# Kernel optimization log

Hardware: AMD Instinct MI355X
Metric: run time of the kernel (lower is better)

The kernel has to match this reference:

```python
import jax, jax.numpy as jnp
import numpy as np

N, L, H, E, V, PAD = 128, 64, 512, 512, 32000, 0


def setup_inputs() -> dict:
    key = jax.random.key(0)
    ks = jax.random.split(key, 8)
    s_in = 1.0 / np.sqrt(E)
    s_sani = 1.0 / np.sqrt(2 * H)
    s_out = 1.0 / np.sqrt(H)
    labels = jax.random.randint(ks[0], (N, L), 0, V)
    emb_table = jax.random.normal(ks[1], (V, E), jnp.float32) * 0.02
    emb_table = emb_table.at[PAD].set(0.0)  # padding_idx row is zero-initialized
    W_in = jax.random.uniform(ks[2], (H, E), jnp.float32, -s_in, s_in)
    b_in = jax.random.uniform(ks[3], (H,), jnp.float32, -s_in, s_in)
    W_sani = jax.random.uniform(ks[4], (H, 2 * H), jnp.float32, -s_sani, s_sani)
    b_sani = jax.random.uniform(ks[5], (H,), jnp.float32, -s_sani, s_sani)
    W_out = jax.random.uniform(ks[6], (E, H), jnp.float32, -s_out, s_out)
    b_out = jax.random.uniform(ks[7], (E,), jnp.float32, -s_out, s_out)
    return dict(labels=labels, emb_table=emb_table, W_in=W_in, b_in=b_in,
                W_sani=W_sani, b_sani=b_sani, W_out=W_out, b_out=b_out)


def reference(labels, emb_table, W_in, b_in, W_sani, b_sani, W_out, b_out):
    n, l = labels.shape
    emb = emb_table[labels]                                   # [N,L,E]
    x = jnp.einsum('nle,he->nlh', emb, W_in) + b_in           # [N,L,H] input conversion
    h_dim = W_in.shape[0]

    def step(states, sc):
        s, h0 = sc                                            # h0: [N,H]
        def body(li, carry):
            h, st = carry
            prev = st[li]                                     # hiddenStateLast[li]
            new_h = jnp.concatenate([prev, h], axis=-1) @ W_sani.T + b_sani
            take = li < s                                     # triangular mask
            return (jnp.where(take, new_h, h),
                    st.at[li].set(jnp.where(take, h, prev)))
        h, states = jax.lax.fori_loop(0, l, body, (h0, states))
        states = states.at[s].set(h)                          # hiddenStateLast[s] = h
        return states, h                                      # outputStates[s] = h

    states0 = jnp.zeros((l, n, h_dim), x.dtype)
    _, outs = jax.lax.scan(step, states0, (jnp.arange(l), jnp.swapaxes(x, 0, 1)))
    # torch: pt.concat(outputStates, dim=0) -> [L*N, H], outputLayer, reshape(N,L,E)
    y = outs.reshape(l * n, h_dim) @ W_out.T + b_out
    y = y.reshape(n, l, E)  # faithful to the original (sequence-major) reshape
    # CrossEntropyLoss with float (probability) targets: classes along dim 1 (L)
    logp = jax.nn.log_softmax(y, axis=1)
    loss = -(emb * logp).sum(axis=1).mean()
    return loss
```

## Files before the change

### kernel.cpp

```cpp
#include <hip/hip_runtime.h>
#include <hip/hip_bf16.h>

typedef __attribute__((ext_vector_type(8))) short short8;
typedef __attribute__((ext_vector_type(4))) float floatx4;

#define NB 128
#define LS 64
#define HD 512
#define ED 512
#define NH 65536
#define LDA 72
#define LDC 136

#define OFF_WIN    0ull
#define OFF_WOUT   524288ull
#define OFF_XT     1048576ull
#define OFF_LVL0   9437184ull
#define OFF_LVL1   17825792ull
#define OFF_OUTS   26214400ull
#define OFF_PA     34603008ull
#define OFF_PB     39845888ull
#define OFF_BCAT   45088768ull
#define OFF_BETA   52428800ull
#define OFF_PART   52436992ull
#define OFF_WSHI   52437504ull
#define OFF_WSLO   53486080ull
#define OFF_PHI    54534656ull
#define OFF_PLO    57156096ull
#define OFF_Y      OFF_LVL0

static __device__ __forceinline__ unsigned short f2b(float f) {
  unsigned u = __float_as_uint(f);
  u += 0x7fffu + ((u >> 16) & 1u);
  return (unsigned short)(u >> 16);
}
static __device__ __forceinline__ float b2f(unsigned short h) {
  return __uint_as_float(((unsigned)h) << 16);
}

static __device__ __forceinline__ void gl_lds16(const unsigned short* g, unsigned short* l) {
  __builtin_amdgcn_global_load_lds(
      (const __attribute__((address_space(1))) void*)g,
      (__attribute__((address_space(3))) void*)l, 16, 0, 0);
}

static __device__ __forceinline__ uint4 cvt8hi(const float* s) {
  floatx4 f0 = *(const floatx4*)s;
  floatx4 f1 = *(const floatx4*)(s + 4);
  float f[8] = {f0.x, f0.y, f0.z, f0.w, f1.x, f1.y, f1.z, f1.w};
  unsigned short b[8];
#pragma unroll
  for (int k = 0; k < 8; ++k) b[k] = f2b(f[k]);
  uint4 u;
  u.x = b[0] | ((unsigned)b[1] << 16); u.y = b[2] | ((unsigned)b[3] << 16);
  u.z = b[4] | ((unsigned)b[5] << 16); u.w = b[6] | ((unsigned)b[7] << 16);
  return u;
}

__device__ __forceinline__ void gemm_core24(const unsigned short* As, const unsigned short* Bs,
                                            floatx4 acc[2][4], int wm, int wn, int lane) {
  const int rb = lane & 15;
  const int kg = (lane >> 4) * 8;
#pragma unroll
  for (int kk = 0; kk < 64; kk += 32) {
    short8 a[2], b[4];
#pragma unroll
    for (int i = 0; i < 2; ++i)
      a[i] = *(const short8*)&As[(wm * 32 + i * 16 + rb) * LDA + kk + kg];
#pragma unroll
    for (int j = 0; j < 4; ++j)
      b[j] = *(const short8*)&Bs[(wn * 64 + j * 16 + rb) * LDA + kk + kg];
#pragma unroll
    for (int i = 0; i < 2; ++i)
#pragma unroll
      for (int j = 0; j < 4; ++j)
        acc[i][j] = __builtin_amdgcn_mfma_f32_16x16x32_bf16(a[i], b[j], acc[i][j], 0, 0, 0);
  }
}

__device__ __forceinline__ void gemm_core64s(const unsigned short* As, const unsigned short* Bs,
                                             floatx4 acc[2][4], int wm, int wn, int lane) {
  const int rb = lane & 15;
  const int kg = (lane >> 4) * 8;
  const int xv = (rb & 7) * 8;
#pragma unroll
  for (int kk = 0; kk < 64; kk += 32) {
    const int co = (kk + kg) ^ xv;
    short8 a[2], b[4];
#pragma unroll
    for (int i = 0; i < 2; ++i)
      a[i] = *(const short8*)&As[(wm * 32 + i * 16 + rb) * 64 + co];
#pragma unroll
    for (int j = 0; j < 4; ++j)
      b[j] = *(const short8*)&Bs[(wn * 64 + j * 16 + rb) * 64 + co];
#pragma unroll
    for (int i = 0; i < 2; ++i)
#pragma unroll
      for (int j = 0; j < 4; ++j)
        acc[i][j] = __builtin_amdgcn_mfma_f32_16x16x32_bf16(a[i], b[j], acc[i][j], 0, 0, 0);
  }
}

__device__ __forceinline__ void stageA_bf16(unsigned short* As, const unsigned short* src, int tid) {
  int r = tid >> 3, kc = (tid & 7) * 8;
#pragma unroll
  for (int p = 0; p < 2; ++p)
    *(uint4*)&As[(r + p * 32) * LDA + kc] = *(const uint4*)(src + (size_t)(r + p * 32) * 512 + kc);
}

__device__ __forceinline__ void stageA_emb(unsigned short* As, const float* table,
                                           const int* labels, int m0, int k0, int tid) {
  int r = tid >> 3, kc = (tid & 7) * 8;
#pragma unroll
  for (int p = 0; p < 2; ++p) {
    int row = r + p * 32;
    const float* s = table + (size_t)labels[m0 + row] * ED + k0 + kc;
    *(uint4*)&As[row * LDA + kc] = cvt8hi(s);
  }
}

__device__ __forceinline__ void stageB(unsigned short* Bs, const unsigned short* src, int ldB, int tid) {
  int r = tid >> 3, kc = (tid & 7) * 8;
#pragma unroll
  for (int p = 0; p < 4; ++p)
    *(uint4*)&Bs[(r + p * 32) * LDA + kc] = *(const uint4*)(src + (size_t)(r + p * 32) * ldB + kc);
}

__global__ __launch_bounds__(256) void k_gemm_emb(const float* __restrict__ table,
                                                  const int* __restrict__ labels,
                                                  const unsigned short* __restrict__ Wb,
                                                  const float* __restrict__ bias,
                                                  unsigned short* __restrict__ xt) {
  __shared__ unsigned short As[64 * LDA];
  __shared__ unsigned short Bs[128 * LDA];
  int tid = threadIdx.x;
  int mtile = blockIdx.x >> 2, ntile = blockIdx.x & 3;
  int m0 = mtile * 64, n0 = ntile * 128;
  int lane = tid & 63, wave = tid >> 6, wm = wave >> 1, wn = wave & 1;
  floatx4 acc[2][4] = {};
  for (int k0 = 0; k0 < 512; k0 += 64) {
    stageA_emb(As, table, labels, m0, k0, tid);
    stageB(Bs, Wb + (size_t)n0 * 512 + k0, 512, tid);
    __syncthreads();
    gemm_core24(As, Bs, acc, wm, wn, lane);
    __syncthreads();
  }
  int rb = lane & 15, rg = (lane >> 4) * 4;
#pragma unroll
  for (int i = 0; i < 2; ++i)
#pragma unroll
    for (int j = 0; j < 4; ++j) {
      int col = n0 + wn * 64 + j * 16 + rb;
      float bv = bias[col];
#pragma unroll
      for (int reg = 0; reg < 4; ++reg) {
        int m = m0 + wm * 32 + i * 16 + rg + reg;
        int n = m >> 6, l = m & 63;
        xt[((size_t)l * NB + n) * HD + col] = f2b(acc[i][j][reg] + bv);
      }
    }
}

__global__ __launch_bounds__(256) void k_cvtWs(const float* __restrict__ Ws,
                                               unsigned short* __restrict__ Hi,
                                               unsigned short* __restrict__ Lo) {
  int i = blockIdx.x * 256 + threadIdx.x;
  const float* s = Ws + (size_t)i * 8;
  unsigned short hb[8], lb[8];
#pragma unroll
  for (int k = 0; k < 8; ++k) {
    float f = s[k];
    unsigned short H = f2b(f);
    hb[k] = H; lb[k] = f2b(f - b2f(H));
  }
  uint4 h, l;
  h.x = hb[0] | ((unsigned)hb[1] << 16); h.y = hb[2] | ((unsigned)hb[3] << 16);
  h.z = hb[4] | ((unsigned)hb[5] << 16); h.w = hb[6] | ((unsigned)hb[7] << 16);
  l.x = lb[0] | ((unsigned)lb[1] << 16); l.y = lb[2] | ((unsigned)lb[3] << 16);
  l.z = lb[4] | ((unsigned)lb[5] << 16); l.w = lb[6] | ((unsigned)lb[7] << 16);
  *(uint4*)(Hi + (size_t)i * 8) = h;
  *(uint4*)(Lo + (size_t)i * 8) = l;
}

__global__ __launch_bounds__(256) void k_cvtP(const float* __restrict__ P,
                                              unsigned short* __restrict__ Hi,
                                              unsigned short* __restrict__ Lo, int n8) {
  int i = blockIdx.x * 256 + threadIdx.x;
  if (i >= n8) return;
  const float* s = P + (size_t)i * 8;
  unsigned short hb[8], lb[8];
#pragma unroll
  for (int k = 0; k < 8; ++k) {
    float f = s[k];
    unsigned short H = f2b(f);
    hb[k] = H; lb[k] = f2b(f - b2f(H));
  }
  uint4 h, l;
  h.x = hb[0] | ((unsigned)hb[1] << 16); h.y = hb[2] | ((unsigned)hb[3] << 16);
  h.z = hb[4] | ((unsigned)hb[5] << 16); h.w = hb[6] | ((unsigned)hb[7] << 16);
  l.x = lb[0] | ((unsigned)lb[1] << 16); l.y = lb[2] | ((unsigned)lb[3] << 16);
  l.z = lb[4] | ((unsigned)lb[5] << 16); l.w = lb[6] | ((unsigned)lb[7] << 16);
  *(uint4*)(Hi + (size_t)i * 8) = h;
  *(uint4*)(Lo + (size_t)i * 8) = l;
}

__global__ __launch_bounds__(256) void k_coef(const unsigned short* __restrict__ Phi,
                                              const unsigned short* __restrict__ Plo,
                                              float* __restrict__ Pout,
                                              const unsigned short* __restrict__ WsHi,
                                              const unsigned short* __restrict__ WsLo,
                                              int m) {
  __shared__ unsigned short As[64 * LDA];
  __shared__ unsigned short Bs[128 * LDA];
  int tid = threadIdx.x;
  int j = blockIdx.x >> 5, tile = blockIdx.x & 31;
  int k0r = (tile >> 2) * 64, n0 = (tile & 3) * 128;
  int lane = tid & 63, wave = tid >> 6, wm = wave >> 1, wn = wave & 1;
  floatx4 acc[2][4] = {};
  for (int term = 0; term < 2; ++term) {
    if (term == 0 && j > m) continue;
    if (term == 1 && j < 1) continue;
    const size_t pbase = (size_t)(term == 0 ? j : j - 1) * 262144;
    const int coloff = (term == 0) ? 512 : 0;
    for (int v = 0; v < 3; ++v) {
      const unsigned short* Asrc = (v == 2 ? Plo : Phi) + pbase;
      const unsigned short* Bsrc = (v == 1 ? WsLo : WsHi);
      for (int t0 = 0; t0 < 512; t0 += 64) {
        stageA_bf16(As, Asrc + (size_t)k0r * 512 + t0, tid);
        stageB(Bs, Bsrc + (size_t)n0 * 1024 + coloff + t0, 1024, tid);
        __syncthreads();
        gemm_core24(As, Bs, acc, wm, wn, lane);
        __syncthreads();
      }
    }
  }
  int rb = lane & 15, rg = (lane >> 4) * 4;
#pragma unroll
  for (int i = 0; i < 2; ++i)
#pragma unroll
    for (int jj = 0; jj < 4; ++jj) {
      int col = n0 + wn * 64 + jj * 16 + rb;
#pragma unroll
      for (int reg = 0; reg < 4; ++reg) {
        int row = wm * 32 + i * 16 + rg + reg;
        Pout[(size_t)j * 262144 + (size_t)(k0r + row) * 512 + col] = acc[i][jj][reg];
      }
    }
}

__global__ __launch_bounds__(256) void k_trW(const float* __restrict__ Ws,
                                             float* __restrict__ P1) {
  __shared__ float t[64][65];
  int mat = blockIdx.x >> 6, tile = blockIdx.x & 63;
  int a0 = (tile >> 3) * 64, b0 = (tile & 7) * 64;
  int coloff = (mat == 0) ? 512 : 0;
  for (int pp = 0; pp < 16; ++pp) {
    int idx = pp * 256 + threadIdx.x, rr = idx >> 6, cc = idx & 63;
    t[rr][cc] = Ws[(size_t)(b0 + rr) * 1024 + coloff + a0 + cc];
  }
  __syncthreads();
  for (int pp = 0; pp < 16; ++pp) {
    int idx = pp * 256 + threadIdx.x, rr = idx >> 6, cc = idx & 63;
    P1[(size_t)mat * 262144 + (size_t)(a0 + rr) * 512 + b0 + cc] = t[cc][rr];
  }
}

__global__ __launch_bounds__(256) void k_trB(const float* __restrict__ Pr,
                                             unsigned short* __restrict__ Bout,
                                             int r) {
  __shared__ float t[64][65];
  int q = blockIdx.x >> 6, tile = blockIdx.x & 63;
  int t0 = (tile >> 3) * 64, i0 = (tile & 7) * 64;
  const float* P = Pr + (size_t)(r - q) * 262144;
  int ldB = (r + 1) * 512;
  for (int pp = 0; pp < 16; ++pp) {
    int idx = pp * 256 + threadIdx.x, rr = idx >> 6, cc = idx & 63;
    t[rr][cc] = P[(size_t)(t0 + rr) * 512 + i0 + cc];
  }
  __syncthreads();
  for (int pp = 0; pp < 16; ++pp) {
    int idx = pp * 256 + threadIdx.x, rr = idx >> 6, cc = idx & 63;
    Bout[(size_t)(i0 + rr) * ldB + q * 512 + t0 + cc] = f2b(t[cc][rr]);
  }
}

__global__ __launch_bounds__(64) void k_bias_step(const float* __restrict__ Ws,
                                                  const float* __restrict__ b,
                                                  const float* __restrict__ bprev,
                                                  float* __restrict__ bout) {
  int i = blockIdx.x, t = threadIdx.x;
  float p = 0.f;
  for (int k = t; k < 512; k += 64)
    p += (Ws[(size_t)i * 1024 + k] + Ws[(size_t)i * 1024 + 512 + k]) * bprev[k];
#pragma unroll
  for (int off = 32; off > 0; off >>= 1) p += __shfl_down(p, off, 64);
  if (t == 0) bout[i] = p + b[i];
}

__global__ __launch_bounds__(256) void k_step(const unsigned short* __restrict__ src,
                                              unsigned short* __restrict__ dst,
                                              unsigned short* __restrict__ outs,
                                              const unsigned short* __restrict__ Bcat,
                                              const float* __restrict__ beta,
                                              int L_prev, int m, int nmain, int g) {
  __shared__ unsigned short lds[24576];
  unsigned short* const A0 = lds;
  unsigned short* const A1 = lds + 4096;
  unsigned short* const B0 = lds + 8192;
  unsigned short* const B1 = lds + 16384;
  const int tid = threadIdx.x, bid = blockIdx.x;
  const int mainWG = 32 * g;
  int r, s, nb0, n0;
  if (bid < mainWG) {
    const int xcd = bid & 7, w = bid >> 3;
    const int sgrp = xcd >> 1, ngrp = xcd & 1;
    const int s_rel = sgrp * g + (w >> 2);
    if (s_rel >= nmain) return;
    const int sub2 = w & 3;
    nb0 = (sub2 >> 1) * 64;
    n0 = (ngrp * 2 + (sub2 & 1)) * 128;
    r = m; s = L_prev + m + s_rel;
  } else {
    const int db = bid - mainWG;
    r = 1 + (db >> 3);
    const int sub = db & 7;
    nb0 = (sub >> 2) * 64; n0 = (sub & 3) * 128;
    s = L_prev + r;
  }
  const int ldB = (r + 1) * 512;
  const unsigned short* Bp = Bcat + (size_t)262144 * (((r - 1) * (r + 2)) >> 1);
  const unsigned short* abase = src + (size_t)(s - r) * NH + (size_t)nb0 * HD;
  const float* bet = beta + (size_t)(r - 1) * 512;
  const int nk = (r + 1) * 8;
  const int lane = tid & 63, wave = tid >> 6, wm = wave >> 1, wn = wave & 1;
  const int rr_ = tid >> 3;
  const int kcs = (((tid & 7) ^ ((tid >> 3) & 7))) * 8;

  floatx4 acc[2][4] = {};

#define STAGE(Ab, Bb, kcol)                                                          \
  { int q_ = (kcol) >> 9, ac_ = (kcol) & 511;                                        \
    const unsigned short* a0_ = abase + (size_t)q_ * NH + ac_;                       \
    unsigned short* lA = (Ab) + (tid >> 6) * 512;                                    \
    unsigned short* lB = (Bb) + (tid >> 6) * 512;                                    \
    gl_lds16(a0_ + (size_t)rr_ * HD + kcs, lA);                                      \
    gl_lds16(a0_ + (size_t)(rr_ + 32) * HD + kcs, lA + 2048);                        \
    gl_lds16(Bp + (size_t)(n0 + rr_) * ldB + (kcol) + kcs, lB);                      \
    gl_lds16(Bp + (size_t)(n0 + rr_ + 32) * ldB + (kcol) + kcs, lB + 2048);          \
    gl_lds16(Bp + (size_t)(n0 + rr_ + 64) * ldB + (kcol) + kcs, lB + 4096);          \
    gl_lds16(Bp + (size_t)(n0 + rr_ + 96) * ldB + (kcol) + kcs, lB + 6144); }

  STAGE(A0, B0, 0)
  __syncthreads();
  for (int k = 0; k < nk; k += 2) {
    if (k + 1 < nk) STAGE(A1, B1, (k + 1) * 64)
    gemm_core64s(A0, B0, acc, wm, wn, lane);
    __syncthreads();
    if (k + 2 < nk) STAGE(A0, B0, (k + 2) * 64)
    gemm_core64s(A1, B1, acc, wm, wn, lane);
    __syncthreads();
  }
#undef STAGE

  unsigned short* Ct = lds;
  const int rbc = lane & 15, rg = (lane >> 4) * 4;
#pragma unroll
  for (int i = 0; i < 2; ++i)
#pragma unroll
    for (int j = 0; j < 4; ++j) {
      int col = wn * 64 + j * 16 + rbc;
      float bv = bet[n0 + col];
#pragma unroll
      for (int reg = 0; reg < 4; ++reg) {
        int row = wm * 32 + i * 16 + rg + reg;
        Ct[row * LDC + col] = f2b(acc[i][j][reg] + bv);
      }
    }
  __syncthreads();
  const bool wdst = (r == m);
  const bool wout = (r < m) || (s == L_prev + m);
  unsigned short* d1 = dst  + (size_t)s * NH + (size_t)nb0 * HD + n0;
  unsigned short* d2 = outs + (size_t)s * NH + (size_t)nb0 * HD + n0;
  const int lrow = tid >> 4, lcol = (tid & 15) * 8;
#pragma unroll
  for (int sweep = 0; sweep < 4; ++sweep) {
    int row = sweep * 16 + lrow;
    uint4 v = *(const uint4*)&Ct[row * LDC + lcol];
    if (wdst) *(uint4*)(d1 + (size_t)row * HD + lcol) = v;
    if (wout) *(uint4*)(d2 + (size_t)row * HD + lcol) = v;
  }
}

__global__ __launch_bounds__(256) void k_gemm_out(const unsigned short* __restrict__ outs,
                                                  const unsigned short* __restrict__ Wb,
                                                  const float* __restrict__ bias,
                                                  float* __restrict__ Y) {
  __shared__ unsigned short As[64 * LDA];
  __shared__ unsigned short Bs[128 * LDA];
  int tid = threadIdx.x;
  int mtile = blockIdx.x >> 2, ntile = blockIdx.x & 3;
  int m0 = mtile * 64, n0 = ntile * 128;
  int lane = tid & 63, wave = tid >> 6, wm = wave >> 1, wn = wave & 1;
  floatx4 acc[2][4] = {};
  for (int k0 = 0; k0 < 512; k0 += 64) {
    stageA_bf16(As, outs + (size_t)m0 * 512 + k0, tid);
    stageB(Bs, Wb + (size_t)n0 * 512 + k0, 512, tid);
    __syncthreads();
    gemm_core24(As, Bs, acc, wm, wn, lane);
    __syncthreads();
  }
  int rb = lane & 15, rg = (lane >> 4) * 4;
#pragma unroll
  for (int i = 0; i < 2; ++i)
#pragma unroll
    for (int j = 0; j < 4; ++j) {
      int col = n0 + wn * 64 + j * 16 + rb;
      float bv = bias[col];
#pragma unroll
      for (int reg = 0; reg < 4; ++reg) {
        int row = m0 + wm * 32 + i * 16 + rg + reg;
        Y[(size_t)row * 512 + col] = acc[i][j][reg] + bv;
      }
    }
}

__global__ __launch_bounds__(256) void k_cvtw(const float* __restrict__ Win,
                                              const float* __restrict__ Wsani,
                                              const float* __restrict__ Wout,
                                              unsigned short* __restrict__ dWin,
                                              unsigned short* __restrict__ dBcat1,
                                              unsigned short* __restrict__ dWout) {
  int i = blockIdx.x * 256 + threadIdx.x;
  const float* src;
  unsigned short* dst;
  int off;
  if (i < 65536)       { src = Win;   dst = dWin;   off = i; }
  else if (i < 196608) { src = Wsani; dst = dBcat1; off = i - 65536; }
  else                 { src = Wout;  dst = dWout;  off = i - 196608; }
  floatx4 v = *(const floatx4*)(src + (size_t)off * 4);
  uint2 u;
  u.x = (unsigned)f2b(v.x) | ((unsigned)f2b(v.y) << 16);
  u.y = (unsigned)f2b(v.z) | ((unsigned)f2b(v.w) << 16);
  *(uint2*)(dst + (size_t)off * 4) = u;
}

__global__ void k_copy(const uint4* __restrict__ src, uint4* __restrict__ dst, int n) {
  int i = blockIdx.x * blockDim.x + threadIdx.x;
  if (i < n) dst[i] = src[i];
}

__global__ __launch_bounds__(256) void k_loss(const float* __restrict__ Y,
                                              const float* __restrict__ table,
                                              const int* __restrict__ labels,
                                              float* __restrict__ partials) {
  int n = blockIdx.x, tid = threadIdx.x;
  float total = 0.f;
#pragma unroll
  for (int e2 = 0; e2 < 2; ++e2) {
    int e = e2 * 256 + tid;
    float mx = -1e30f;
    for (int l = 0; l < 64; ++l)
      mx = fmaxf(mx, Y[(size_t)(n * 64 + l) * 512 + e]);
    float se = 0.f;
    for (int l = 0; l < 64; ++l)
      se += expf(Y[(size_t)(n * 64 + l) * 512 + e] - mx);
    float lse = mx + logf(se);
    for (int l = 0; l < 64; ++l) {
      float embv = table[(size_t)labels[n * 64 + l] * ED + e];
      total += embv * (Y[(size_t)(n * 64 + l) * 512 + e] - lse);
    }
  }
  __shared__ float red[256];
  red[tid] = total;
  __syncthreads();
  for (int s2 = 128; s2 > 0; s2 >>= 1) {
    if (tid < s2) red[tid] += red[tid + s2];
    __syncthreads();
  }
  if (tid == 0) partials[n] = red[0];
}

__global__ void k_final(const float* __restrict__ partials, float* __restrict__ out) {
  if (threadIdx.x == 0) {
    double s = 0.0;
    for (int i = 0; i < 128; ++i) s += (double)partials[i];
    out[0] = (float)(-s / 65536.0);
  }
}

extern "C" void kernel_launch(void* const* d_in, const int* in_sizes, int n_in,
                              void* d_out, int out_size, void* d_ws, size_t ws_size,
                              hipStream_t stream) {
  const int*   labels = (const int*)d_in[0];
  const float* table  = (const float*)d_in[1];
  const float* W_in   = (const float*)d_in[2];
  const float* b_in   = (const float*)d_in[3];
  const float* W_sani = (const float*)d_in[4];
  const float* b_sani = (const float*)d_in[5];
  const float* W_out  = (const float*)d_in[6];
  const float* b_out  = (const float*)d_in[7];

  char* ws = (char*)d_ws;
  unsigned short* Win_b  = (unsigned short*)(ws + OFF_WIN);
  unsigned short* Wout_b = (unsigned short*)(ws + OFF_WOUT);
  unsigned short* xt     = (unsigned short*)(ws + OFF_XT);
  unsigned short* lvl0   = (unsigned short*)(ws + OFF_LVL0);
  unsigned short* lvl1   = (unsigned short*)(ws + OFF_LVL1);
  unsigned short* outs   = (unsigned short*)(ws + OFF_OUTS);
  float*          Pa     = (float*)(ws + OFF_PA);
  float*          Pb     = (float*)(ws + OFF_PB);
  unsigned short* Bcat   = (unsigned short*)(ws + OFF_BCAT);
  float*          beta   = (float*)(ws + OFF_BETA);
  float*          parts  = (float*)(ws + OFF_PART);
  unsigned short* WsHi   = (unsigned short*)(ws + OFF_WSHI);
  unsigned short* WsLo   = (unsigned short*)(ws + OFF_WSLO);
  unsigned short* PHi    = (unsigned short*)(ws + OFF_PHI);
  unsigned short* PLo    = (unsigned short*)(ws + OFF_PLO);
  float*          Y      = (float*)(ws + OFF_Y);

  k_cvtw<<<1024, 256, 0, stream>>>(W_in, W_sani, W_out, Win_b, Bcat, Wout_b);
  k_cvtWs<<<256, 256, 0, stream>>>(W_sani, WsHi, WsLo);
  k_gemm_emb<<<512, 256, 0, stream>>>(table, labels, Win_b, b_in, xt);
  k_copy<<<32, 256, 0, stream>>>((const uint4*)xt, (uint4*)outs, 8192);

  k_copy<<<1, 128, 0, stream>>>((const uint4*)b_sani, (uint4*)beta, 128);
  k_bias_step<<<512, 64, 0, stream>>>(W_sani, b_sani, beta,        beta + 512);
  k_bias_step<<<512, 64, 0, stream>>>(W_sani, b_sani, beta + 512,  beta + 1024);
  k_bias_step<<<512, 64, 0, stream>>>(W_sani, b_sani, beta + 1024, beta + 1536);

  k_trW <<<128, 256, 0, stream>>>(W_sani, Pa);
  k_cvtP<<<256, 256, 0, stream>>>(Pa, PHi, PLo, 65536);
  k_coef<<< 96, 256, 0, stream>>>(PHi, PLo, Pb, WsHi, WsLo, 1);
  k_cvtP<<<384, 256, 0, stream>>>(Pb, PHi, PLo, 98304);
  k_trB <<<192, 256, 0, stream>>>(Pb, Bcat + 524288, 2);
  k_coef<<<128, 256, 0, stream>>>(PHi, PLo, Pa, WsHi, WsLo, 2);
  k_cvtP<<<512, 256, 0, stream>>>(Pa, PHi, PLo, 131072);
  k_trB <<<256, 256, 0, stream>>>(Pa, Bcat + 1310720, 3);
  k_coef<<<160, 256, 0, stream>>>(PHi, PLo, Pb, WsHi, WsLo, 3);
  k_trB <<<320, 256, 0, stream>>>(Pb, Bcat + 2359296, 4);

  const unsigned short* srcp = xt;
  for (int j = 1; j <= 16; ++j) {
    int L_prev = 4 * (j - 1);
    int m = (j == 16) ? 3 : 4;
    int nmain = 64 - (L_prev + m);
    int g = (nmain + 3) >> 2;
    unsigned short* dstp = ((j - 1) & 1) ? lvl1 : lvl0;
    k_step<<<32 * g + (m - 1) * 8, 256, 0, stream>>>(srcp, dstp, outs, Bcat, beta,
                                                     L_prev, m, nmain, g);
    srcp = dstp;
  }

  k_gemm_out<<<512, 256, 0, stream>>>(outs, Wout_b, b_out, Y);
  k_loss<<<128, 256, 0, stream>>>(Y, table, labels, parts);
  k_final<<<1, 64, 0, stream>>>(parts, (float*)d_out);
}
```

Baseline: 628.7 us.

## Fuse precompute conversions, double-buffer coef and output GEMMs, merge bias kernels

Folds the hi/lo bf16 split of W_sani into the weight-conversion kernel and produces hi/lo P matrices directly in k_trW and k_coef epilogues, which removes the separate k_cvtWs and k_cvtP launches and the fp32 P round trips. WsHi is now read from Bcat. The three bias-step launches are merged into one single-block kernel. k_coef and k_gemm_out now stage tiles with double-buffered direct global-to-LDS loads and a swizzled core, and the output GEMM writes Y through an LDS-staged coalesced epilogue. This cuts launch count and memory traffic in the setup phase, but the single-block bias kernel runs serially.

```diff
diff --git a/kernel.cpp b/kernel.cpp
--- a/kernel.cpp
+++ b/kernel.cpp
@@ -11,6 +11,7 @@
 #define NH 65536
 #define LDA 72
 #define LDC 136
+#define LDCF 132
 
 #define OFF_WIN    0ull
 #define OFF_WOUT   524288ull
@@ -18,15 +19,14 @@
 #define OFF_LVL0   9437184ull
 #define OFF_LVL1   17825792ull
 #define OFF_OUTS   26214400ull
-#define OFF_PA     34603008ull
-#define OFF_PB     39845888ull
+#define OFF_PHA    34603008ull
+#define OFF_PLA    37224448ull
+#define OFF_PHB    39845888ull
+#define OFF_PLB    42467328ull
 #define OFF_BCAT   45088768ull
 #define OFF_BETA   52428800ull
 #define OFF_PART   52436992ull
-#define OFF_WSHI   52437504ull
-#define OFF_WSLO   53486080ull
-#define OFF_PHI    54534656ull
-#define OFF_PLO    57156096ull
+#define OFF_WSLO   52437504ull
 #define OFF_Y      OFF_LVL0
 
 static __device__ __forceinline__ unsigned short f2b(float f) {
@@ -99,13 +99,6 @@
       for (int j = 0; j < 4; ++j)
         acc[i][j] = __builtin_amdgcn_mfma_f32_16x16x32_bf16(a[i], b[j], acc[i][j], 0, 0, 0);
   }
-}
-
-__device__ __forceinline__ void stageA_bf16(unsigned short* As, const unsigned short* src, int tid) {
-  int r = tid >> 3, kc = (tid & 7) * 8;
-#pragma unroll
-  for (int p = 0; p < 2; ++p)
-    *(uint4*)&As[(r + p * 32) * LDA + kc] = *(const uint4*)(src + (size_t)(r + p * 32) * 512 + kc);
 }
 
 __device__ __forceinline__ void stageA_emb(unsigned short* As, const float* table,
@@ -161,95 +154,44 @@
     }
 }
 
-__global__ __launch_bounds__(256) void k_cvtWs(const float* __restrict__ Ws,
-                                               unsigned short* __restrict__ Hi,
-                                               unsigned short* __restrict__ Lo) {
+__global__ __launch_bounds__(256) void k_cvtw(const float* __restrict__ Win,
+                                              const float* __restrict__ Wsani,
+                                              const float* __restrict__ Wout,
+                                              unsigned short* __restrict__ dWin,
+                                              unsigned short* __restrict__ dBcat1,
+                                              unsigned short* __restrict__ dWsLo,
+                                              unsigned short* __restrict__ dWout) {
   int i = blockIdx.x * 256 + threadIdx.x;
-  const float* s = Ws + (size_t)i * 8;
-  unsigned short hb[8], lb[8];
-#pragma unroll
-  for (int k = 0; k < 8; ++k) {
-    float f = s[k];
-    unsigned short H = f2b(f);
-    hb[k] = H; lb[k] = f2b(f - b2f(H));
-  }
-  uint4 h, l;
-  h.x = hb[0] | ((unsigned)hb[1] << 16); h.y = hb[2] | ((unsigned)hb[3] << 16);
-  h.z = hb[4] | ((unsigned)hb[5] << 16); h.w = hb[6] | ((unsigned)hb[7] << 16);
-  l.x = lb[0] | ((unsigned)lb[1] << 16); l.y = lb[2] | ((unsigned)lb[3] << 16);
-  l.z = lb[4] | ((unsigned)lb[5] << 16); l.w = lb[6] | ((unsigned)lb[7] << 16);
-  *(uint4*)(Hi + (size_t)i * 8) = h;
-  *(uint4*)(Lo + (size_t)i * 8) = l;
-}
-
-__global__ __launch_bounds__(256) void k_cvtP(const float* __restrict__ P,
-                                              unsigned short* __restrict__ Hi,
-                                              unsigned short* __restrict__ Lo, int n8) {
-  int i = blockIdx.x * 256 + threadIdx.x;
-  if (i >= n8) return;
-  const float* s = P + (size_t)i * 8;
-  unsigned short hb[8], lb[8];
-#pragma unroll
-  for (int k = 0; k < 8; ++k) {
-    float f = s[k];
-    unsigned short H = f2b(f);
-    hb[k] = H; lb[k] = f2b(f - b2f(H));
-  }
-  uint4 h, l;
-  h.x = hb[0] | ((unsigned)hb[1] << 16); h.y = hb[2] | ((unsigned)hb[3] << 16);
-  h.z = hb[4] | ((unsigned)hb[5] << 16); h.w = hb[6] | ((unsigned)hb[7] << 16);
-  l.x = lb[0] | ((unsigned)lb[1] << 16); l.y = lb[2] | ((unsigned)lb[3] << 16);
-  l.z = lb[4] | ((unsigned)lb[5] << 16); l.w = lb[6] | ((unsigned)lb[7] << 16);
-  *(uint4*)(Hi + (size_t)i * 8) = h;
-  *(uint4*)(Lo + (size_t)i * 8) = l;
-}
-
-__global__ __launch_bounds__(256) void k_coef(const unsigned short* __restrict__ Phi,
-                                              const unsigned short* __restrict__ Plo,
-                                              float* __restrict__ Pout,
-                                              const unsigned short* __restrict__ WsHi,
-                                              const unsigned short* __restrict__ WsLo,
-                                              int m) {
-  __shared__ unsigned short As[64 * LDA];
-  __shared__ unsigned short Bs[128 * LDA];
-  int tid = threadIdx.x;
-  int j = blockIdx.x >> 5, tile = blockIdx.x & 31;
-  int k0r = (tile >> 2) * 64, n0 = (tile & 3) * 128;
-  int lane = tid & 63, wave = tid >> 6, wm = wave >> 1, wn = wave & 1;
-  floatx4 acc[2][4] = {};
-  for (int term = 0; term < 2; ++term) {
-    if (term == 0 && j > m) continue;
-    if (term == 1 && j < 1) continue;
-    const size_t pbase = (size_t)(term == 0 ? j : j - 1) * 262144;
-    const int coloff = (term == 0) ? 512 : 0;
-    for (int v = 0; v < 3; ++v) {
-      const unsigned short* Asrc = (v == 2 ? Plo : Phi) + pbase;
-      const unsigned short* Bsrc = (v == 1 ? WsLo : WsHi);
-      for (int t0 = 0; t0 < 512; t0 += 64) {
-        stageA_bf16(As, Asrc + (size_t)k0r * 512 + t0, tid);
-        stageB(Bs, Bsrc + (size_t)n0 * 1024 + coloff + t0, 1024, tid);
-        __syncthreads();
-        gemm_core24(As, Bs, acc, wm, wn, lane);
-        __syncthreads();
-      }
-    }
-  }
-  int rb = lane & 15, rg = (lane >> 4) * 4;
-#pragma unroll
-  for (int i = 0; i < 2; ++i)
-#pragma unroll
-    for (int jj = 0; jj < 4; ++jj) {
-      int col = n0 + wn * 64 + jj * 16 + rb;
-#pragma unroll
-      for (int reg = 0; reg < 4; ++reg) {
-        int row = wm * 32 + i * 16 + rg + reg;
-        Pout[(size_t)j * 262144 + (size_t)(k0r + row) * 512 + col] = acc[i][jj][reg];
-      }
-    }
+  if (i < 65536 || i >= 196608) {
+    const float* src = (i < 65536) ? Win : Wout;
+    unsigned short* dst = (i < 65536) ? dWin : dWout;
+    int off = (i < 65536) ? i : i - 196608;
+    floatx4 v = *(const floatx4*)(src + (size_t)off * 4);
+    uint2 u;
+    u.x = (unsigned)f2b(v.x) | ((unsigned)f2b(v.y) << 16);
+    u.y = (unsigned)f2b(v.z) | ((unsigned)f2b(v.w) << 16);
+    *(uint2*)(dst + (size_t)off * 4) = u;
+  } else {
+    int off = i - 65536;
+    floatx4 v = *(const floatx4*)(Wsani + (size_t)off * 4);
+    float f[4] = {v.x, v.y, v.z, v.w};
+    unsigned short hb[4], lb[4];
+#pragma unroll
+    for (int k = 0; k < 4; ++k) {
+      hb[k] = f2b(f[k]);
+      lb[k] = f2b(f[k] - b2f(hb[k]));
+    }
+    uint2 h, l;
+    h.x = hb[0] | ((unsigned)hb[1] << 16); h.y = hb[2] | ((unsigned)hb[3] << 16);
+    l.x = lb[0] | ((unsigned)lb[1] << 16); l.y = lb[2] | ((unsigned)lb[3] << 16);
+    *(uint2*)(dBcat1 + (size_t)off * 4) = h;
+    *(uint2*)(dWsLo + (size_t)off * 4) = l;
+  }
 }
 
 __global__ __launch_bounds__(256) void k_trW(const float* __restrict__ Ws,
-                                             float* __restrict__ P1) {
+                                             unsigned short* __restrict__ Phi,
+                                             unsigned short* __restrict__ Plo) {
   __shared__ float t[64][65];
   int mat = blockIdx.x >> 6, tile = blockIdx.x & 63;
   int a0 = (tile >> 3) * 64, b0 = (tile & 7) * 64;
@@ -261,17 +203,92 @@
   __syncthreads();
   for (int pp = 0; pp < 16; ++pp) {
     int idx = pp * 256 + threadIdx.x, rr = idx >> 6, cc = idx & 63;
-    P1[(size_t)mat * 262144 + (size_t)(a0 + rr) * 512 + b0 + cc] = t[cc][rr];
-  }
-}
-
-__global__ __launch_bounds__(256) void k_trB(const float* __restrict__ Pr,
+    float f = t[cc][rr];
+    unsigned short hi = f2b(f);
+    size_t o = (size_t)mat * 262144 + (size_t)(a0 + rr) * 512 + b0 + cc;
+    Phi[o] = hi;
+    Plo[o] = f2b(f - b2f(hi));
+  }
+}
+
+__global__ __launch_bounds__(256) void k_coef(const unsigned short* __restrict__ Phi,
+                                              const unsigned short* __restrict__ Plo,
+                                              unsigned short* __restrict__ PhiOut,
+                                              unsigned short* __restrict__ PloOut,
+                                              const unsigned short* __restrict__ WsHi,
+                                              const unsigned short* __restrict__ WsLo,
+                                              int m) {
+  __shared__ unsigned short lds[24576];
+  unsigned short* const A0 = lds;
+  unsigned short* const A1 = lds + 4096;
+  unsigned short* const B0 = lds + 8192;
+  unsigned short* const B1 = lds + 16384;
+  const int tid = threadIdx.x;
+  const int j = blockIdx.x >> 5, tile = blockIdx.x & 31;
+  const int k0r = (tile >> 2) * 64, n0 = (tile & 3) * 128;
+  const int lane = tid & 63, wave = tid >> 6, wm = wave >> 1, wn = wave & 1;
+  const int rr_ = tid >> 3;
+  const int kcs = (((tid & 7) ^ ((tid >> 3) & 7))) * 8;
+  const int t_first = (j <= m) ? 0 : 1;
+  const int nterms = ((j <= m) ? 1 : 0) + ((j >= 1) ? 1 : 0);
+  const int nsteps = nterms * 24;
+
+  floatx4 acc[2][4] = {};
+
+#define STAGE_C(Ab, Bb, u)                                                           \
+  { int term_ = t_first + (((u) >= 24) ? 1 : 0);                                     \
+    int v_ = ((u) >> 3) % 3;                                                         \
+    int t0_ = ((u) & 7) * 64;                                                        \
+    const unsigned short* As_ = ((v_ == 2) ? Plo : Phi)                              \
+        + (size_t)(term_ ? (j - 1) : j) * 262144 + (size_t)k0r * 512 + t0_;          \
+    const unsigned short* Bs_ = ((v_ == 1) ? WsLo : WsHi)                            \
+        + (size_t)n0 * 1024 + (term_ ? 0 : 512) + t0_;                               \
+    unsigned short* lA = (Ab) + (tid >> 6) * 512;                                    \
+    unsigned short* lB = (Bb) + (tid >> 6) * 512;                                    \
+    gl_lds16(As_ + (size_t)rr_ * 512 + kcs, lA);                                     \
+    gl_lds16(As_ + (size_t)(rr_ + 32) * 512 + kcs, lA + 2048);                       \
+    gl_lds16(Bs_ + (size_t)rr_ * 1024 + kcs, lB);                                    \
+    gl_lds16(Bs_ + (size_t)(rr_ + 32) * 1024 + kcs, lB + 2048);                      \
+    gl_lds16(Bs_ + (size_t)(rr_ + 64) * 1024 + kcs, lB + 4096);                      \
+    gl_lds16(Bs_ + (size_t)(rr_ + 96) * 1024 + kcs, lB + 6144); }
+
+  STAGE_C(A0, B0, 0)
+  __syncthreads();
+  for (int u = 0; u < nsteps; u += 2) {
+    if (u + 1 < nsteps) STAGE_C(A1, B1, u + 1)
+    gemm_core64s(A0, B0, acc, wm, wn, lane);
+    __syncthreads();
+    if (u + 2 < nsteps) STAGE_C(A0, B0, u + 2)
+    gemm_core64s(A1, B1, acc, wm, wn, lane);
+    __syncthreads();
+  }
+#undef STAGE_C
+
+  const int rb = lane & 15, rg = (lane >> 4) * 4;
+#pragma unroll
+  for (int i = 0; i < 2; ++i)
+#pragma unroll
+    for (int jj = 0; jj < 4; ++jj) {
+      int col = n0 + wn * 64 + jj * 16 + rb;
+#pragma unroll
+      for (int reg = 0; reg < 4; ++reg) {
+        int row = wm * 32 + i * 16 + rg + reg;
+        float f = acc[i][jj][reg];
+        unsigned short hi = f2b(f);
+        size_t o = (size_t)j * 262144 + (size_t)(k0r + row) * 512 + col;
+        PhiOut[o] = hi;
+        PloOut[o] = f2b(f - b2f(hi));
+      }
+    }
+}
+
+__global__ __launch_bounds__(256) void k_trB(const unsigned short* __restrict__ Phi,
                                              unsigned short* __restrict__ Bout,
                                              int r) {
-  __shared__ float t[64][65];
+  __shared__ unsigned short t[64][68];
   int q = blockIdx.x >> 6, tile = blockIdx.x & 63;
   int t0 = (tile >> 3) * 64, i0 = (tile & 7) * 64;
-  const float* P = Pr + (size_t)(r - q) * 262144;
+  const unsigned short* P = Phi + (size_t)(r - q) * 262144;
   int ldB = (r + 1) * 512;
   for (int pp = 0; pp < 16; ++pp) {
     int idx = pp * 256 + threadIdx.x, rr = idx >> 6, cc = idx & 63;
@@ -280,21 +297,34 @@
   __syncthreads();
   for (int pp = 0; pp < 16; ++pp) {
     int idx = pp * 256 + threadIdx.x, rr = idx >> 6, cc = idx & 63;
-    Bout[(size_t)(i0 + rr) * ldB + q * 512 + t0 + cc] = f2b(t[cc][rr]);
-  }
-}
-
-__global__ __launch_bounds__(64) void k_bias_step(const float* __restrict__ Ws,
+    Bout[(size_t)(i0 + rr) * ldB + q * 512 + t0 + cc] = t[cc][rr];
+  }
+}
+
+__global__ __launch_bounds__(512) void k_bias_all(const float* __restrict__ Ws,
                                                   const float* __restrict__ b,
-                                                  const float* __restrict__ bprev,
-                                                  float* __restrict__ bout) {
-  int i = blockIdx.x, t = threadIdx.x;
-  float p = 0.f;
-  for (int k = t; k < 512; k += 64)
-    p += (Ws[(size_t)i * 1024 + k] + Ws[(size_t)i * 1024 + 512 + k]) * bprev[k];
-#pragma unroll
-  for (int off = 32; off > 0; off >>= 1) p += __shfl_down(p, off, 64);
-  if (t == 0) bout[i] = p + b[i];
+                                                  float* __restrict__ beta) {
+  __shared__ float bprev[512];
+  __shared__ float bnext[512];
+  const int tid = threadIdx.x, g = tid >> 6, lane = tid & 63;
+  bprev[tid] = b[tid];
+  beta[tid] = b[tid];
+  __syncthreads();
+  for (int step = 1; step <= 3; ++step) {
+    for (int oi = 0; oi < 64; ++oi) {
+      int i = oi * 8 + g;
+      float p = 0.f;
+      for (int k = lane; k < 512; k += 64)
+        p += (Ws[(size_t)i * 1024 + k] + Ws[(size_t)i * 1024 + 512 + k]) * bprev[k];
+#pragma unroll
+      for (int off = 32; off > 0; off >>= 1) p += __shfl_down(p, off, 64);
+      if (lane == 0) bnext[i] = p + b[i];
+    }
+    __syncthreads();
+    bprev[tid] = bnext[tid];
+    beta[step * 512 + tid] = bnext[tid];
+    __syncthreads();
+  }
 }
 
 __global__ __launch_bounds__(256) void k_step(const unsigned short* __restrict__ src,
@@ -395,53 +425,66 @@
                                                   const unsigned short* __restrict__ Wb,
                                                   const float* __restrict__ bias,
                                                   float* __restrict__ Y) {
-  __shared__ unsigned short As[64 * LDA];
-  __shared__ unsigned short Bs[128 * LDA];
-  int tid = threadIdx.x;
-  int mtile = blockIdx.x >> 2, ntile = blockIdx.x & 3;
-  int m0 = mtile * 64, n0 = ntile * 128;
-  int lane = tid & 63, wave = tid >> 6, wm = wave >> 1, wn = wave & 1;
+  __shared__ unsigned short lds[24576];
+  unsigned short* const A0 = lds;
+  unsigned short* const A1 = lds + 4096;
+  unsigned short* const B0 = lds + 8192;
+  unsigned short* const B1 = lds + 16384;
+  const int tid = threadIdx.x;
+  const int mtile = blockIdx.x >> 2, ntile = blockIdx.x & 3;
+  const int m0 = mtile * 64, n0 = ntile * 128;
+  const int lane = tid & 63, wave = tid >> 6, wm = wave >> 1, wn = wave & 1;
+  const int rr_ = tid >> 3;
+  const int kcs = (((tid & 7) ^ ((tid >> 3) & 7))) * 8;
+  const unsigned short* abase = outs + (size_t)m0 * 512;
+  const unsigned short* Bp = Wb + (size_t)n0 * 512;
+
   floatx4 acc[2][4] = {};
-  for (int k0 = 0; k0 < 512; k0 += 64) {
-    stageA_bf16(As, outs + (size_t)m0 * 512 + k0, tid);
-    stageB(Bs, Wb + (size_t)n0 * 512 + k0, 512, tid);
-    __syncthreads();
-    gemm_core24(As, Bs, acc, wm, wn, lane);
-    __syncthreads();
-  }
-  int rb = lane & 15, rg = (lane >> 4) * 4;
+
+#define STAGE_O(Ab, Bb, kcol)                                                        \
+  { unsigned short* lA = (Ab) + (tid >> 6) * 512;                                    \
+    unsigned short* lB = (Bb) + (tid >> 6) * 512;                                    \
+    gl_lds16(abase + (size_t)rr_ * 512 + (kcol) + kcs, lA);                          \
+    gl_lds16(abase + (size_t)(rr_ + 32) * 512 + (kcol) + kcs, lA + 2048);            \
+    gl_lds16(Bp + (size_t)rr_ * 512 + (kcol) + kcs, lB);                             \
+    gl_lds16(Bp + (size_t)(rr_ + 32) * 512 + (kcol) + kcs, lB + 2048);               \
+    gl_lds16(Bp + (size_t)(rr_ + 64) * 512 + (kcol) + kcs, lB + 4096);               \
+    gl_lds16(Bp + (size_t)(rr_ + 96) * 512 + (kcol) + kcs, lB + 6144); }
+
+  STAGE_O(A0, B0, 0)
+  __syncthreads();
+  for (int k = 0; k < 8; k += 2) {
+    if (k + 1 < 8) STAGE_O(A1, B1, (k + 1) * 64)
+    gemm_core64s(A0, B0, acc, wm, wn, lane);
+    __syncthreads();
+    if (k + 2 < 8) STAGE_O(A0, B0, (k + 2) * 64)
+    gemm_core64s(A1, B1, acc, wm, wn, lane);
+    __syncthreads();
+  }
+#undef STAGE_O
+
+  float* Ctf = (float*)lds;
+  const int rbc = lane & 15, rg = (lane >> 4) * 4;
 #pragma unroll
   for (int i = 0; i < 2; ++i)
 #pragma unroll
     for (int j = 0; j < 4; ++j) {
-      int col = n0 + wn * 64 + j * 16 + rb;
-      float bv = bias[col];
+      int col = wn * 64 + j * 16 + rbc;
+      float bv = bias[n0 + col];
 #pragma unroll
       for (int reg = 0; reg < 4; ++reg) {
-        int row = m0 + wm * 32 + i * 16 + rg + reg;
-        Y[(size_t)row * 512 + col] = acc[i][j][reg] + bv;
+        int row = wm * 32 + i * 16 + rg + reg;
+        Ctf[row * LDCF + col] = acc[i][j][reg] + bv;
       }
     }
-}
-
-__global__ __launch_bounds__(256) void k_cvtw(const float* __restrict__ Win,
-                                              const float* __restrict__ Wsani,
-                                              const float* __restrict__ Wout,
-                                              unsigned short* __restrict__ dWin,
-                                              unsigned short* __restrict__ dBcat1,
-                                              unsigned short* __restrict__ dWout) {
-  int i = blockIdx.x * 256 + threadIdx.x;
-  const float* src;
-  unsigned short* dst;
-  int off;
-  if (i < 65536)       { src = Win;   dst = dWin;   off = i; }
-  else if (i < 196608) { src = Wsani; dst = dBcat1; off = i - 65536; }
-  else                 { src = Wout;  dst = dWout;  off = i - 196608; }
-  floatx4 v = *(const floatx4*)(src + (size_t)off * 4);
-  uint2 u;
-  u.x = (unsigned)f2b(v.x) | ((unsigned)f2b(v.y) << 16);
-  u.y = (unsigned)f2b(v.z) | ((unsigned)f2b(v.w) << 16);
-  *(uint2*)(dst + (size_t)off * 4) = u;
+  __syncthreads();
+  const int lrow = tid >> 5, lc = (tid & 31) * 4;
+#pragma unroll
+  for (int sweep = 0; sweep < 8; ++sweep) {
+    int row = sweep * 8 + lrow;
+    uint4 v = *(const uint4*)&Ctf[row * LDCF + lc];
+    *(uint4*)&Y[(size_t)(m0 + row) * 512 + n0 + lc] = v;
+  }
 }
 
 __global__ void k_copy(const uint4* __restrict__ src, uint4* __restrict__ dst, int n) {
@@ -507,37 +550,28 @@
   unsigned short* lvl0   = (unsigned short*)(ws + OFF_LVL0);
   unsigned short* lvl1   = (unsigned short*)(ws + OFF_LVL1);
   unsigned short* outs   = (unsigned short*)(ws + OFF_OUTS);
-  float*          Pa     = (float*)(ws + OFF_PA);
-  float*          Pb     = (float*)(ws + OFF_PB);
+  unsigned short* PhiA   = (unsigned short*)(ws + OFF_PHA);
+  unsigned short* PloA   = (unsigned short*)(ws + OFF_PLA);
+  unsigned short* PhiB   = (unsigned short*)(ws + OFF_PHB);
+  unsigned short* PloB   = (unsigned short*)(ws + OFF_PLB);
   unsigned short* Bcat   = (unsigned short*)(ws + OFF_BCAT);
   float*          beta   = (float*)(ws + OFF_BETA);
   float*          parts  = (float*)(ws + OFF_PART);
-  unsigned short* WsHi   = (unsigned short*)(ws + OFF_WSHI);
   unsigned short* WsLo   = (unsigned short*)(ws + OFF_WSLO);
-  unsigned short* PHi    = (unsigned short*)(ws + OFF_PHI);
-  unsigned short* PLo    = (unsigned short*)(ws + OFF_PLO);
   float*          Y      = (float*)(ws + OFF_Y);
 
-  k_cvtw<<<1024, 256, 0, stream>>>(W_in, W_sani, W_out, Win_b, Bcat, Wout_b);
-  k_cvtWs<<<256, 256, 0, stream>>>(W_sani, WsHi, WsLo);
+  k_cvtw<<<1024, 256, 0, stream>>>(W_in, W_sani, W_out, Win_b, Bcat, WsLo, Wout_b);
   k_gemm_emb<<<512, 256, 0, stream>>>(table, labels, Win_b, b_in, xt);
   k_copy<<<32, 256, 0, stream>>>((const uint4*)xt, (uint4*)outs, 8192);
-
-  k_copy<<<1, 128, 0, stream>>>((const uint4*)b_sani, (uint4*)beta, 128);
-  k_bias_step<<<512, 64, 0, stream>>>(W_sani, b_sani, beta,        beta + 512);
-  k_bias_step<<<512, 64, 0, stream>>>(W_sani, b_sani, beta + 512,  beta + 1024);
-  k_bias_step<<<512, 64, 0, stream>>>(W_sani, b_sani, beta + 1024, beta + 1536);
-
-  k_trW <<<128, 256, 0, stream>>>(W_sani, Pa);
-  k_cvtP<<<256, 256, 0, stream>>>(Pa, PHi, PLo, 65536);
-  k_coef<<< 96, 256, 0, stream>>>(PHi, PLo, Pb, WsHi, WsLo, 1);
-  k_cvtP<<<384, 256, 0, stream>>>(Pb, PHi, PLo, 98304);
-  k_trB <<<192, 256, 0, stream>>>(Pb, Bcat + 524288, 2);
-  k_coef<<<128, 256, 0, stream>>>(PHi, PLo, Pa, WsHi, WsLo, 2);
-  k_cvtP<<<512, 256, 0, stream>>>(Pa, PHi, PLo, 131072);
-  k_trB <<<256, 256, 0, stream>>>(Pa, Bcat + 1310720, 3);
-  k_coef<<<160, 256, 0, stream>>>(PHi, PLo, Pb, WsHi, WsLo, 3);
-  k_trB <<<320, 256, 0, stream>>>(Pb, Bcat + 2359296, 4);
+  k_bias_all<<<1, 512, 0, stream>>>(W_sani, b_sani, beta);
+
+  k_trW <<<128, 256, 0, stream>>>(W_sani, PhiA, PloA);
+  k_coef<<< 96, 256, 0, stream>>>(PhiA, PloA, PhiB, PloB, Bcat, WsLo, 1);
+  k_trB <<<192, 256, 0, stream>>>(PhiB, Bcat + 524288, 2);
+  k_coef<<<128, 256, 0, stream>>>(PhiB, PloB, PhiA, PloA, Bcat, WsLo, 2);
+  k_trB <<<256, 256, 0, stream>>>(PhiA, Bcat + 1310720, 3);
+  k_coef<<<160, 256, 0, stream>>>(PhiA, PloA, PhiB, PloB, Bcat, WsLo, 3);
+  k_trB <<<320, 256, 0, stream>>>(PhiB, Bcat + 2359296, 4);
 
   const unsigned short* srcp = xt;
   for (int j = 1; j <= 16; ++j) {
```

Result: slower. 688.3 us (+9.5%).
